# Kernel tuning notes

Hardware: AMD Instinct MI355X
Metric: run time of the kernel (lower is better)

## Reference

```python
import jax, jax.numpy as jnp
import numpy as np

N = 100_000          # nodes
E = 3_200_000        # edges (avg degree 32)
USER_SIZE = 80_000
CAT_SIZE = 5_000
USER_DIM = 8
CAT_DIM = 4
IN_CH = 8
OUT_CH = 16
HID = 16


def setup_inputs() -> dict:
    key = jax.random.key(0)
    ks = jax.random.split(key, 24)
    # features: [N,3] int; col0 = id (user id if type==0 else category id), col1 = known flag in {0,1}, col2 = type in {0,1}
    typ = jax.random.randint(ks[0], (N,), 0, 2)
    uid = jax.random.randint(ks[1], (N,), 0, USER_SIZE)
    cid = jax.random.randint(ks[2], (N,), 0, CAT_SIZE)
    col0 = jnp.where(typ == 0, uid, cid)
    col1 = jax.random.randint(ks[3], (N,), 0, 2)
    features = jnp.stack([col0, col1, typ], axis=1).astype(jnp.int64)
    edges = jax.random.randint(ks[4], (2, E), 0, N).astype(jnp.int64)

    def p(k, shape):
        return jax.random.normal(k, shape, dtype=jnp.float32) * 0.1

    return {
        "edges": edges,
        "features": features,
        "emb_user": p(ks[5], (USER_SIZE, USER_DIM)),
        "emb_known": p(ks[6], (2, USER_DIM)),
        "w_user": p(ks[7], (USER_DIM, IN_CH)),
        "b_user": p(ks[8], (IN_CH,)),
        "emb_cat": p(ks[9], (CAT_SIZE, CAT_DIM)),
        "w_cat": p(ks[10], (CAT_DIM, IN_CH)),
        "b_cat": p(ks[11], (IN_CH,)),
        "w0": p(ks[12], (IN_CH, HID)),
        "b0": p(ks[13], (HID,)),
        "w2": p(ks[14], (HID, OUT_CH)),
        "b2": p(ks[15], (OUT_CH,)),
        "w_node": p(ks[16], (OUT_CH, 2)),
        "b_node": p(ks[17], (2,)),
        "w_mem": p(ks[18], (OUT_CH, 1)),
        "b_mem": p(ks[19], (1,)),
    }


def _gcn_conv(x, w, b, src, dst, edge_norm, self_norm, n):
    h = x @ w                                      # [N, out]
    msgs = h[src] * edge_norm[:, None]             # [E, out] gather + scale
    agg = jax.ops.segment_sum(msgs, dst, num_segments=n)  # scatter-add
    agg = agg + h * self_norm[:, None]             # self-loop term
    return agg + b


def reference(edges, features, emb_user, emb_known, w_user, b_user, emb_cat,
              w_cat, b_cat, w0, b0, w2, b2, w_node, b_node, w_mem, b_mem):
    n = features.shape[0]
    typ = features[:, -1]
    is_user = (typ == 0)

    # --- input encoding (masked gather/scatter expressed as dense select) ---
    uidx = jnp.clip(features[:, 0], 0, emb_user.shape[0] - 1)
    kidx = jnp.clip(features[:, 1], 0, 1)
    cidx = jnp.clip(features[:, 0], 0, emb_cat.shape[0] - 1)
    user_f = jax.nn.relu(emb_user[uidx] + emb_known[kidx]) @ w_user + b_user
    cat_f = jax.nn.relu(emb_cat[cidx]) @ w_cat + b_cat
    x = jnp.where(is_user[:, None], user_f, cat_f)  # [N, IN_CH]

    # --- GCN normalization (shared across layers) ---
    src, dst = edges[0], edges[1]
    deg = jax.ops.segment_sum(jnp.ones((src.shape[0],), x.dtype), dst,
                              num_segments=n) + 1.0  # +1 for self-loop
    dinv = jax.lax.rsqrt(deg)
    edge_norm = dinv[src] * dinv[dst]
    self_norm = dinv * dinv

    # NOTE: original forward loop skips layers[1] entirely (enumerate over layers[:-2],
    # then applies layers[-1]); dropout branch (i>1) never triggers. Faithful here.
    h = jax.nn.relu(_gcn_conv(x, w0, b0, src, dst, edge_norm, self_norm, n))
    h = jax.nn.relu(_gcn_conv(h, w2, b2, src, dst, edge_norm, self_norm, n))

    member_pred = h @ w_mem + b_mem   # [N, 1]
    node_pred = h @ w_node + b_node   # [N, 2]
    return (member_pred, node_pred)
```

## Files before the change

kernel.cpp:

```cpp
#include <hip/hip_runtime.h>
#include <hip/hip_fp16.h>

#define BLK 256
#define PBLK 1024
#define NPB 256
#define CSHIFT 10
#define CNODES 1024
#define CMASK 1023
#define NBCMAX 128
#define CAP 40960
#define SSHIFT 6
#define NSL 16
#define SROWS 64
#define SRMASK 63
#define NCHK 8
#define FCAP2 384
#define FXS 1048576.0f
#define FXI (1.0f / 1048576.0f)
#define PBIAS (1 << 23)

typedef int v4i __attribute__((ext_vector_type(4)));
typedef unsigned long long u64;

static inline int cdiv(int a, int b) { return (a + b - 1) / b; }

__global__ void __launch_bounds__(PBLK)
k_hist(const int* __restrict__ dst, int* __restrict__ histG, int e, int nb) {
    __shared__ int h[4][NBCMAX];
    int tid = threadIdx.x;
    int rep = (tid >> 6) & 3;
    for (int t = tid; t < 4 * NBCMAX; t += PBLK) ((int*)h)[t] = 0;
    __syncthreads();
    int per = ((e + (int)gridDim.x - 1) / (int)gridDim.x + 3) & ~3;
    int beg = blockIdx.x * per;
    int end = min(e, beg + per);
    if (beg < end) {
        int m4 = beg + ((end - beg) & ~3);
        for (int i = beg + tid * 4; i < m4; i += PBLK * 4) {
            v4i d4 = __builtin_nontemporal_load((const v4i*)(dst + i));
            atomicAdd(&h[rep][d4[0] >> CSHIFT], 1);
            atomicAdd(&h[rep][d4[1] >> CSHIFT], 1);
            atomicAdd(&h[rep][d4[2] >> CSHIFT], 1);
            atomicAdd(&h[rep][d4[3] >> CSHIFT], 1);
        }
        int it = m4 + tid;
        if (it < end) atomicAdd(&h[rep][dst[it] >> CSHIFT], 1);
    }
    __syncthreads();
    for (int t = tid; t < nb; t += PBLK)
        histG[(size_t)blockIdx.x * nb + t] = h[0][t] + h[1][t] + h[2][t] + h[3][t];
}

__global__ void __launch_bounds__(NPB)
k_base(const int* __restrict__ histG, int* __restrict__ baseG, int* __restrict__ tot, int nb) {
    __shared__ int s[NPB];
    int b = blockIdx.x;
    int t = threadIdx.x;
    int hc = histG[(size_t)t * nb + b];
    int r = (hc + 15) & ~15;
    s[t] = r;
    __syncthreads();
    for (int off = 1; off < NPB; off <<= 1) {
        int v = (t >= off) ? s[t - off] : 0;
        __syncthreads();
        s[t] += v;
        __syncthreads();
    }
    int excl = s[t] - r;
    baseG[(size_t)t * nb + b] = b * CAP + excl;
    if (t == NPB - 1) tot[b] = min(s[t], CAP);
}

__global__ void __launch_bounds__(PBLK)
k_scatter(const int* __restrict__ src, const int* __restrict__ dst,
          const int* __restrict__ baseG, int* __restrict__ slab, int e, int nb) {
    __shared__ int cur[NBCMAX];
    int tid = threadIdx.x;
    int blk = blockIdx.x;
    for (int t = tid; t < nb; t += PBLK) cur[t] = baseG[(size_t)blk * nb + t];
    __syncthreads();
    int per = ((e + (int)gridDim.x - 1) / (int)gridDim.x + 3) & ~3;
    int beg = blk * per;
    int end = min(e, beg + per);
    if (beg < end) {
        int m4 = beg + ((end - beg) & ~3);
        for (int i = beg + tid * 4; i < m4; i += PBLK * 4) {
            v4i s4 = __builtin_nontemporal_load((const v4i*)(src + i));
            v4i d4 = __builtin_nontemporal_load((const v4i*)(dst + i));
#pragma unroll
            for (int k = 0; k < 4; ++k) {
                int d = d4[k];
                int b = d >> CSHIFT;
                int pos = atomicAdd(&cur[b], 1);
                if (pos < (b + 1) * CAP) slab[pos] = (s4[k] << CSHIFT) | (d & CMASK);
            }
        }
        int it = m4 + tid;
        if (it < end) {
            int d = dst[it];
            int b = d >> CSHIFT;
            int pos = atomicAdd(&cur[b], 1);
            if (pos < (b + 1) * CAP) slab[pos] = (src[it] << CSHIFT) | (d & CMASK);
        }
    }
    __syncthreads();
    for (int bb = tid; bb < nb; bb += PBLK) {
        int c = cur[bb];
        int lim = (bb + 1) * CAP;
        while ((c & 15) && c < lim) slab[c++] = -1;
    }
}

__global__ void __launch_bounds__(PBLK)
k_refine(const int* __restrict__ tot, const int* __restrict__ cslab,
         int* __restrict__ fslab, int* __restrict__ ftot,
         int* __restrict__ deg, int n) {
    __shared__ int cur[NSL];
    __shared__ int cnt[CNODES];
    int tid = threadIdx.x;
    int b = blockIdx.x >> 3;
    int p = blockIdx.x & 7;
    if (tid < NSL) cur[tid] = 0;
    for (int t = tid; t < CNODES; t += PBLK) cnt[t] = 0;
    __syncthreads();
    int nlines = tot[b] >> 4;
    int q0 = ((p * nlines) >> 3) << 2;
    int q1 = (((p + 1) * nlines) >> 3) << 2;
    const v4i* sl4 = reinterpret_cast<const v4i*>(cslab + (size_t)b * CAP);
    for (int i = q0 + tid; i < q1; i += PBLK) {
        v4i e4 = sl4[i];
#pragma unroll
        for (int k = 0; k < 4; ++k) {
            int e = e4[k];
            if (e >= 0) {
                int s = (e >> SSHIFT) & (NSL - 1);
                int fe = ((e >> CSHIFT) << SSHIFT) | (e & SRMASK);
                atomicAdd(&cnt[e & CMASK], 1);
                int pos = atomicAdd(&cur[s], 1);
                if (pos < FCAP2) fslab[(size_t)((b * NSL + s) * NCHK + p) * FCAP2 + pos] = fe;
            }
        }
    }
    __syncthreads();
    if (tid < NSL) {
        int cc = min(cur[tid], FCAP2);
        int r = min((cc + 15) & ~15, FCAP2);
        int* seg = fslab + (size_t)((b * NSL + tid) * NCHK + p) * FCAP2;
        for (int x = cc; x < r; ++x) seg[x] = -1;
        ftot[(b * NSL + tid) * NCHK + p] = r;
    }
    for (int t = tid; t < CNODES; t += PBLK) {
        int v = cnt[t];
        int nd = b * CNODES + t;
        if (v && nd < n) atomicAdd(&deg[nd], v);
    }
}

__global__ void k_featmm(const int* __restrict__ feat,
                         const float* __restrict__ emb_user,
                         const float* __restrict__ emb_known,
                         const float* __restrict__ w_user,
                         const float* __restrict__ b_user,
                         const float* __restrict__ emb_cat,
                         const float* __restrict__ w_cat,
                         const float* __restrict__ b_cat,
                         const float* __restrict__ w0,
                         const int* __restrict__ deg,
                         __half* __restrict__ Hs,
                         int n, int user_max, int cat_max) {
    __shared__ float w0s[8 * 16];
    for (int t = threadIdx.x; t < 8 * 16; t += blockDim.x) w0s[t] = w0[t];
    __syncthreads();
    int i = blockIdx.x * blockDim.x + threadIdx.x;
    if (i >= n) return;
    int col0 = feat[i * 3 + 0];
    int col1 = feat[i * 3 + 1];
    int typ  = feat[i * 3 + 2];
    float x[8];
    if (typ == 0) {
        int u = min(max(col0, 0), user_max);
        int k = min(max(col1, 0), 1);
        const float4* eu = reinterpret_cast<const float4*>(emb_user + (size_t)u * 8);
        const float4* ek = reinterpret_cast<const float4*>(emb_known + (size_t)k * 8);
        float4 a0 = eu[0], a1 = eu[1], k0 = ek[0], k1 = ek[1];
        float in[8];
        in[0] = fmaxf(a0.x + k0.x, 0.f); in[1] = fmaxf(a0.y + k0.y, 0.f);
        in[2] = fmaxf(a0.z + k0.z, 0.f); in[3] = fmaxf(a0.w + k0.w, 0.f);
        in[4] = fmaxf(a1.x + k1.x, 0.f); in[5] = fmaxf(a1.y + k1.y, 0.f);
        in[6] = fmaxf(a1.z + k1.z, 0.f); in[7] = fmaxf(a1.w + k1.w, 0.f);
#pragma unroll
        for (int c = 0; c < 8; ++c) {
            float s = b_user[c];
#pragma unroll
            for (int d = 0; d < 8; ++d) s += in[d] * w_user[d * 8 + c];
            x[c] = s;
        }
    } else {
        int ci = min(max(col0, 0), cat_max);
        float4 c0 = reinterpret_cast<const float4*>(emb_cat + (size_t)ci * 4)[0];
        float in[4];
        in[0] = fmaxf(c0.x, 0.f); in[1] = fmaxf(c0.y, 0.f);
        in[2] = fmaxf(c0.z, 0.f); in[3] = fmaxf(c0.w, 0.f);
#pragma unroll
        for (int c = 0; c < 8; ++c) {
            float s = b_cat[c];
#pragma unroll
            for (int d = 0; d < 4; ++d) s += in[d] * w_cat[d * 8 + c];
            x[c] = s;
        }
    }
    float dv = rsqrtf((float)deg[i] + 1.0f);
    float o[16];
#pragma unroll
    for (int c = 0; c < 16; ++c) {
        float s = 0.f;
#pragma unroll
        for (int d = 0; d < 8; ++d) s += x[d] * w0s[d * 16 + c];
        o[c] = s * dv;
    }
    union { __half2 h[8]; uint4 u[2]; } pk;
#pragma unroll
    for (int k = 0; k < 8; ++k) pk.h[k] = __floats2half2_rn(o[2 * k], o[2 * k + 1]);
    uint4* dp = reinterpret_cast<uint4*>(Hs + (size_t)i * 16);
    dp[0] = pk.u[0];
    dp[1] = pk.u[1];
}

__device__ __forceinline__ void gather_pair(const int* __restrict__ run0, int n0,
                                            const int* __restrict__ run1, int n1,
                                            const uint4* __restrict__ Hs4,
                                            u64 (*acc64)[9], int tid) {
    const v4i* sl0 = reinterpret_cast<const v4i*>(run0);
    const v4i* sl1 = reinterpret_cast<const v4i*>(run1);
    int ns0 = n0 >> 2, ns1 = n1 >> 2;
    int maxs = max(ns0, ns1);
    int g = tid >> 1, q = tid & 1;
    for (int base = 0; base < maxs; base += 128) {
        int i = base + g;
        v4i e0 = sl0[min(i, (FCAP2 >> 2) - 1)];
        v4i e1 = sl1[min(i, (FCAP2 >> 2) - 1)];
        bool b0 = i < ns0, b1 = i < ns1;
        int us[8];
        us[0] = b0 ? e0[0] : -1; us[1] = b0 ? e0[1] : -1;
        us[2] = b0 ? e0[2] : -1; us[3] = b0 ? e0[3] : -1;
        us[4] = b1 ? e1[0] : -1; us[5] = b1 ? e1[1] : -1;
        us[6] = b1 ? e1[2] : -1; us[7] = b1 ? e1[3] : -1;
        uint4 v[8];
#pragma unroll
        for (int k = 0; k < 8; ++k)
            if (us[k] >= 0) v[k] = Hs4[(size_t)(us[k] >> SSHIFT) * 2 + q];
#pragma unroll
        for (int k = 0; k < 8; ++k) {
            if (us[k] >= 0) {
                int dl = us[k] & SRMASK;
                union { uint4 u4; __half2 h[4]; } c;
                c.u4 = v[k];
#pragma unroll
                for (int j = 0; j < 4; ++j) {
                    float2 f = __half22float2(c.h[j]);
                    unsigned a0 = (unsigned)(__float2int_rn(f.x * FXS) + PBIAS);
                    unsigned a1 = (unsigned)(__float2int_rn(f.y * FXS) + PBIAS);
                    u64 pk = ((u64)a1 << 32) | (u64)a0;
                    atomicAdd(&acc64[dl][q * 4 + j], pk);
                }
            }
        }
    }
}

__device__ __forceinline__ void gather_fb(const int* __restrict__ ftot,
                                          const int* __restrict__ fslab,
                                          int fb, const uint4* __restrict__ Hs4,
                                          u64 (*acc64)[9], int tid) {
#pragma unroll
    for (int p = 0; p < NCHK; p += 2) {
        const int* r0 = fslab + (size_t)(fb * NCHK + p) * FCAP2;
        const int* r1 = fslab + (size_t)(fb * NCHK + p + 1) * FCAP2;
        gather_pair(r0, ftot[fb * NCHK + p], r1, ftot[fb * NCHK + p + 1], Hs4, acc64, tid);
    }
}

__device__ __forceinline__ float unpack_acc(const u64 (*acc64)[9], int node, int c, int dg) {
    u64 w = acc64[node][c >> 1];
    unsigned raw = (c & 1) ? (unsigned)(w >> 32) : (unsigned)(w & 0xffffffffULL);
    long long t = (long long)raw - (long long)dg * PBIAS;
    return (float)t * FXI;
}

__global__ void __launch_bounds__(BLK, 8)
k_bconv1(const int* __restrict__ ftot, const int* __restrict__ fslab,
         const __half* __restrict__ Hs, const int* __restrict__ deg,
         const float* __restrict__ b0, const float* __restrict__ w2,
         __half* __restrict__ Hs2, int n) {
    __shared__ u64 acc64[SROWS][9];
    __shared__ float w2s[16 * 16];
    __shared__ float b0s[16];
    int tid = threadIdx.x;
    for (int t = tid; t < SROWS * 9; t += BLK) ((u64*)acc64)[t] = 0ull;
    w2s[tid] = w2[tid];
    if (tid < 16) b0s[tid] = b0[tid];
    __syncthreads();
    int fb = blockIdx.x;
    gather_fb(ftot, fslab, fb, reinterpret_cast<const uint4*>(Hs), acc64, tid);
    __syncthreads();
    int node = tid & 63;
    int qq = tid >> 6;
    int nd = (fb >> 4) * CNODES + (fb & (NSL - 1)) * SROWS + node;
    if (nd < n) {
        int dg = deg[nd];
        float dv = rsqrtf((float)dg + 1.0f);
        const __half* hrow = Hs + (size_t)nd * 16;
        float h1[16];
#pragma unroll
        for (int c = 0; c < 16; ++c) {
            float v = dv * (unpack_acc(acc64, node, c, dg) + __half2float(hrow[c])) + b0s[c];
            h1[c] = v > 0.f ? v : 0.f;
        }
        float o[4];
#pragma unroll
        for (int j = 0; j < 4; ++j) {
            float sum = 0.f;
#pragma unroll
            for (int c = 0; c < 16; ++c) sum += h1[c] * w2s[c * 16 + qq * 4 + j];
            o[j] = sum * dv;
        }
        union { __half2 h[2]; uint2 u; } pk;
        pk.h[0] = __floats2half2_rn(o[0], o[1]);
        pk.h[1] = __floats2half2_rn(o[2], o[3]);
        *reinterpret_cast<uint2*>(Hs2 + (size_t)nd * 16 + qq * 4) = pk.u;
    }
}

__global__ void __launch_bounds__(BLK, 8)
k_bconv2(const int* __restrict__ ftot, const int* __restrict__ fslab,
         const __half* __restrict__ Hs, const int* __restrict__ deg,
         const float* __restrict__ b2,
         const float* __restrict__ w_mem, const float* __restrict__ b_mem,
         const float* __restrict__ w_node, const float* __restrict__ b_node,
         float* __restrict__ out, int n) {
    __shared__ u64 acc64[SROWS][9];
    __shared__ float wms[16], wn0[16], wn1[16], b2s[16];
    int tid = threadIdx.x;
    for (int t = tid; t < SROWS * 9; t += BLK) ((u64*)acc64)[t] = 0ull;
    if (tid < 16) {
        wms[tid] = w_mem[tid];
        wn0[tid] = w_node[tid * 2 + 0];
        wn1[tid] = w_node[tid * 2 + 1];
        b2s[tid] = b2[tid];
    }
    __syncthreads();
    int fb = blockIdx.x;
    gather_fb(ftot, fslab, fb, reinterpret_cast<const uint4*>(Hs), acc64, tid);
    __syncthreads();
    int nd = (fb >> 4) * CNODES + (fb & (NSL - 1)) * SROWS + tid;
    if (tid < SROWS && nd < n) {
        int dg = deg[nd];
        float dv = rsqrtf((float)dg + 1.0f);
        const __half* hrow = Hs + (size_t)nd * 16;
        float mph = b_mem[0];
        float n0 = b_node[0];
        float n1 = b_node[1];
#pragma unroll
        for (int c = 0; c < 16; ++c) {
            float v = dv * (unpack_acc(acc64, tid, c, dg) + __half2float(hrow[c])) + b2s[c];
            float h = v > 0.f ? v : 0.f;
            mph += h * wms[c];
            n0  += h * wn0[c];
            n1  += h * wn1[c];
        }
        out[nd] = mph;
        out[n + 2 * nd + 0] = n0;
        out[n + 2 * nd + 1] = n1;
    }
}

extern "C" void kernel_launch(void* const* d_in, const int* in_sizes, int n_in,
                              void* d_out, int out_size, void* d_ws, size_t ws_size,
                              hipStream_t stream) {
    const int*   edges     = (const int*)d_in[0];
    const int*   feat      = (const int*)d_in[1];
    const float* emb_user  = (const float*)d_in[2];
    const float* emb_known = (const float*)d_in[3];
    const float* w_user    = (const float*)d_in[4];
    const float* b_user    = (const float*)d_in[5];
    const float* emb_cat   = (const float*)d_in[6];
    const float* w_cat     = (const float*)d_in[7];
    const float* b_cat     = (const float*)d_in[8];
    const float* w0        = (const float*)d_in[9];
    const float* b0        = (const float*)d_in[10];
    const float* w2        = (const float*)d_in[11];
    const float* b2        = (const float*)d_in[12];
    const float* w_node    = (const float*)d_in[13];
    const float* b_node    = (const float*)d_in[14];
    const float* w_mem     = (const float*)d_in[15];
    const float* b_mem     = (const float*)d_in[16];

    const int E = in_sizes[0] / 2;
    const int n = in_sizes[1] / 3;
    const int user_max = in_sizes[2] / 8 - 1;
    const int cat_max  = in_sizes[6] / 4 - 1;
    const int NBC = cdiv(n, CNODES);
    const int NBF = NBC * NSL;

    const int* src = edges;
    const int* dst = edges + E;

    int* cslab   = (int*)d_ws;
    int* fslab   = cslab + (size_t)NBC * CAP;
    __half* hsA  = (__half*)(fslab + (size_t)NBF * NCHK * FCAP2);
    __half* hsB  = hsA + (size_t)n * 16;
    int* histG   = (int*)(hsB + (size_t)n * 16);
    int* baseG   = histG + (size_t)NPB * NBC;
    int* tot     = baseG + (size_t)NPB * NBC;
    int* deg     = tot + NBC;
    int* ftot    = deg + n;

    float* outp = (float*)d_out;

    hipMemsetAsync(deg, 0, (size_t)n * sizeof(int), stream);
    k_hist<<<NPB, PBLK, 0, stream>>>(dst, histG, E, NBC);
    k_base<<<NBC, NPB, 0, stream>>>(histG, baseG, tot, NBC);
    k_scatter<<<NPB, PBLK, 0, stream>>>(src, dst, baseG, cslab, E, NBC);
    k_refine<<<NBC * NCHK, PBLK, 0, stream>>>(tot, cslab, fslab, ftot, deg, n);
    k_featmm<<<cdiv(n, BLK), BLK, 0, stream>>>(feat, emb_user, emb_known, w_user, b_user,
                                               emb_cat, w_cat, b_cat, w0, deg, hsA,
                                               n, user_max, cat_max);
    k_bconv1<<<NBF, BLK, 0, stream>>>(ftot, fslab, hsA, deg, b0, w2, hsB, n);
    k_bconv2<<<NBF, BLK, 0, stream>>>(ftot, fslab, hsB, deg, b2,
                                      w_mem, b_mem, w_node, b_node, outp, n);
}
```

Before: 108.4 us.

## Fuse histogram, prefix-scan and scatter into one partition kernel using global atomics

Three kernels (block histogram, per-bucket prefix scan, scatter) become one partition kernel. Each block counts its edges per coarse bucket in shared memory, reserves a 16-aligned range in each bucket's slab with a global atomicAdd, then scatters into it and pads the leftover with -1. This removes two launches and the histogram/base round trips through global memory, and it reuses the dst reads while they are hot in cache. In exchange, slab order within a bucket now depends on scheduling, the loads are no longer nontemporal, and the refine kernel clamps the bucket total to CAP.

```diff
diff --git a/kernel.cpp b/kernel.cpp
--- a/kernel.cpp
+++ b/kernel.cpp
@@ -25,11 +25,14 @@
 static inline int cdiv(int a, int b) { return (a + b - 1) / b; }
 
 __global__ void __launch_bounds__(PBLK)
-k_hist(const int* __restrict__ dst, int* __restrict__ histG, int e, int nb) {
-    __shared__ int h[4][NBCMAX];
+k_part(const int* __restrict__ src, const int* __restrict__ dst,
+       int* __restrict__ gcur, int* __restrict__ slab, int e, int nb) {
+    __shared__ int hist[4][NBCMAX];
+    __shared__ int curs[NBCMAX];
+    __shared__ int rend[NBCMAX];
     int tid = threadIdx.x;
     int rep = (tid >> 6) & 3;
-    for (int t = tid; t < 4 * NBCMAX; t += PBLK) ((int*)h)[t] = 0;
+    for (int t = tid; t < 4 * NBCMAX; t += PBLK) ((int*)hist)[t] = 0;
     __syncthreads();
     int per = ((e + (int)gridDim.x - 1) / (int)gridDim.x + 3) & ~3;
     int beg = blockIdx.x * per;
@@ -37,77 +40,51 @@
     if (beg < end) {
         int m4 = beg + ((end - beg) & ~3);
         for (int i = beg + tid * 4; i < m4; i += PBLK * 4) {
-            v4i d4 = __builtin_nontemporal_load((const v4i*)(dst + i));
-            atomicAdd(&h[rep][d4[0] >> CSHIFT], 1);
-            atomicAdd(&h[rep][d4[1] >> CSHIFT], 1);
-            atomicAdd(&h[rep][d4[2] >> CSHIFT], 1);
-            atomicAdd(&h[rep][d4[3] >> CSHIFT], 1);
+            v4i d4 = *reinterpret_cast<const v4i*>(dst + i);
+            atomicAdd(&hist[rep][d4[0] >> CSHIFT], 1);
+            atomicAdd(&hist[rep][d4[1] >> CSHIFT], 1);
+            atomicAdd(&hist[rep][d4[2] >> CSHIFT], 1);
+            atomicAdd(&hist[rep][d4[3] >> CSHIFT], 1);
         }
         int it = m4 + tid;
-        if (it < end) atomicAdd(&h[rep][dst[it] >> CSHIFT], 1);
-    }
-    __syncthreads();
-    for (int t = tid; t < nb; t += PBLK)
-        histG[(size_t)blockIdx.x * nb + t] = h[0][t] + h[1][t] + h[2][t] + h[3][t];
-}
-
-__global__ void __launch_bounds__(NPB)
-k_base(const int* __restrict__ histG, int* __restrict__ baseG, int* __restrict__ tot, int nb) {
-    __shared__ int s[NPB];
-    int b = blockIdx.x;
-    int t = threadIdx.x;
-    int hc = histG[(size_t)t * nb + b];
-    int r = (hc + 15) & ~15;
-    s[t] = r;
-    __syncthreads();
-    for (int off = 1; off < NPB; off <<= 1) {
-        int v = (t >= off) ? s[t - off] : 0;
-        __syncthreads();
-        s[t] += v;
-        __syncthreads();
-    }
-    int excl = s[t] - r;
-    baseG[(size_t)t * nb + b] = b * CAP + excl;
-    if (t == NPB - 1) tot[b] = min(s[t], CAP);
-}
-
-__global__ void __launch_bounds__(PBLK)
-k_scatter(const int* __restrict__ src, const int* __restrict__ dst,
-          const int* __restrict__ baseG, int* __restrict__ slab, int e, int nb) {
-    __shared__ int cur[NBCMAX];
-    int tid = threadIdx.x;
-    int blk = blockIdx.x;
-    for (int t = tid; t < nb; t += PBLK) cur[t] = baseG[(size_t)blk * nb + t];
-    __syncthreads();
-    int per = ((e + (int)gridDim.x - 1) / (int)gridDim.x + 3) & ~3;
-    int beg = blk * per;
-    int end = min(e, beg + per);
+        if (it < end) atomicAdd(&hist[rep][dst[it] >> CSHIFT], 1);
+    }
+    __syncthreads();
+    for (int b = tid; b < nb; b += PBLK) {
+        int cnt = hist[0][b] + hist[1][b] + hist[2][b] + hist[3][b];
+        int r16 = (cnt + 15) & ~15;
+        int base = 0;
+        if (r16) base = atomicAdd(&gcur[b], r16);
+        int a0 = b * CAP + min(base, CAP);
+        int a1 = b * CAP + min(base + r16, CAP);
+        curs[b] = a0;
+        rend[b] = a1;
+    }
+    __syncthreads();
     if (beg < end) {
         int m4 = beg + ((end - beg) & ~3);
         for (int i = beg + tid * 4; i < m4; i += PBLK * 4) {
-            v4i s4 = __builtin_nontemporal_load((const v4i*)(src + i));
-            v4i d4 = __builtin_nontemporal_load((const v4i*)(dst + i));
+            v4i s4 = *reinterpret_cast<const v4i*>(src + i);
+            v4i d4 = *reinterpret_cast<const v4i*>(dst + i);
 #pragma unroll
             for (int k = 0; k < 4; ++k) {
                 int d = d4[k];
                 int b = d >> CSHIFT;
-                int pos = atomicAdd(&cur[b], 1);
-                if (pos < (b + 1) * CAP) slab[pos] = (s4[k] << CSHIFT) | (d & CMASK);
+                int pos = atomicAdd(&curs[b], 1);
+                if (pos < rend[b]) slab[pos] = (s4[k] << CSHIFT) | (d & CMASK);
             }
         }
         int it = m4 + tid;
         if (it < end) {
             int d = dst[it];
             int b = d >> CSHIFT;
-            int pos = atomicAdd(&cur[b], 1);
-            if (pos < (b + 1) * CAP) slab[pos] = (src[it] << CSHIFT) | (d & CMASK);
-        }
-    }
-    __syncthreads();
-    for (int bb = tid; bb < nb; bb += PBLK) {
-        int c = cur[bb];
-        int lim = (bb + 1) * CAP;
-        while ((c & 15) && c < lim) slab[c++] = -1;
+            int pos = atomicAdd(&curs[b], 1);
+            if (pos < rend[b]) slab[pos] = (src[it] << CSHIFT) | (d & CMASK);
+        }
+    }
+    __syncthreads();
+    for (int b = tid; b < nb; b += PBLK) {
+        for (int x = curs[b]; x < rend[b]; ++x) slab[x] = -1;
     }
 }
 
@@ -123,7 +100,7 @@
     if (tid < NSL) cur[tid] = 0;
     for (int t = tid; t < CNODES; t += PBLK) cnt[t] = 0;
     __syncthreads();
-    int nlines = tot[b] >> 4;
+    int nlines = min(tot[b], CAP) >> 4;
     int q0 = ((p * nlines) >> 3) << 2;
     int q1 = (((p + 1) * nlines) >> 3) << 2;
     const v4i* sl4 = reinterpret_cast<const v4i*>(cslab + (size_t)b * CAP);
@@ -409,19 +386,15 @@
     int* fslab   = cslab + (size_t)NBC * CAP;
     __half* hsA  = (__half*)(fslab + (size_t)NBF * NCHK * FCAP2);
     __half* hsB  = hsA + (size_t)n * 16;
-    int* histG   = (int*)(hsB + (size_t)n * 16);
-    int* baseG   = histG + (size_t)NPB * NBC;
-    int* tot     = baseG + (size_t)NPB * NBC;
-    int* deg     = tot + NBC;
+    int* gcur    = (int*)(hsB + (size_t)n * 16);
+    int* deg     = gcur + NBC;
     int* ftot    = deg + n;
 
     float* outp = (float*)d_out;
 
-    hipMemsetAsync(deg, 0, (size_t)n * sizeof(int), stream);
-    k_hist<<<NPB, PBLK, 0, stream>>>(dst, histG, E, NBC);
-    k_base<<<NBC, NPB, 0, stream>>>(histG, baseG, tot, NBC);
-    k_scatter<<<NPB, PBLK, 0, stream>>>(src, dst, baseG, cslab, E, NBC);
-    k_refine<<<NBC * NCHK, PBLK, 0, stream>>>(tot, cslab, fslab, ftot, deg, n);
+    hipMemsetAsync(gcur, 0, (size_t)(NBC + n) * sizeof(int), stream);
+    k_part<<<NPB, PBLK, 0, stream>>>(src, dst, gcur, cslab, E, NBC);
+    k_refine<<<NBC * NCHK, PBLK, 0, stream>>>(gcur, cslab, fslab, ftot, deg, n);
     k_featmm<<<cdiv(n, BLK), BLK, 0, stream>>>(feat, emb_user, emb_known, w_user, b_user,
                                                emb_cat, w_cat, b_cat, w0, deg, hsA,
                                                n, user_max, cat_max);
```

New measurement: 101.0 us (median of 2 runs). -6.8%, faster.
